# Performance work log

Measured on AMD Instinct MI355X. Metric: run time of the kernel, lower is better.

Reference implementation:

```python
import jax, jax.numpy as jnp
import numpy as np
from math import sqrt

I, H, O = 1024, 1024, 1024

def setup_inputs() -> dict:
    key = jax.random.key(0)
    ks = jax.random.split(key, 11)
    sx = sqrt(2.0 / (I + H))
    sh = sqrt(1.0 / H)
    sy = sqrt(2.0 / (H + O))
    return {
        "x": jax.random.normal(ks[0], (64, 512, I), dtype=jnp.float32),
        "W_xi": jax.random.normal(ks[1], (I, H), dtype=jnp.float32) * sx,
        "W_hi": jax.random.normal(ks[2], (H, H), dtype=jnp.float32) * sh,
        "b_i": jnp.zeros((H,), jnp.float32),
        "W_xf": jax.random.normal(ks[3], (I, H), dtype=jnp.float32) * sx,
        "W_hf": jax.random.normal(ks[4], (H, H), dtype=jnp.float32) * sh,
        "b_f": jnp.zeros((H,), jnp.float32),
        "W_xo": jax.random.normal(ks[5], (I, H), dtype=jnp.float32) * sx,
        "W_ho": jax.random.normal(ks[6], (H, H), dtype=jnp.float32) * sh,
        "b_o": jnp.zeros((H,), jnp.float32),
        "W_xc": jax.random.normal(ks[7], (I, H), dtype=jnp.float32) * sx,
        "W_hc": jax.random.normal(ks[8], (H, H), dtype=jnp.float32) * sh,
        "b_c": jnp.zeros((H,), jnp.float32),
        "W_hy": jax.random.normal(ks[9], (H, O), dtype=jnp.float32) * sy,
        "b_y": jnp.zeros((O,), jnp.float32),
    }

def reference(x, W_xi, W_hi, b_i, W_xf, W_hf, b_f, W_xo, W_ho, b_o,
              W_xc, W_hc, b_c, W_hy, b_y):
    B, T, _ = x.shape
    Hs = W_hi.shape[0]
    # Precompute all input-to-gate projections in one batched GEMM per gate.
    # Shapes: [B, T, H]
    xi = jnp.einsum('bti,ih->bth', x, W_xi) + b_i
    xf = jnp.einsum('bti,ih->bth', x, W_xf) + b_f
    xo = jnp.einsum('bti,ih->bth', x, W_xo) + b_o
    xc = jnp.einsum('bti,ih->bth', x, W_xc) + b_c

    def step(carry, inp):
        h, c = carry
        xi_t, xf_t, xo_t, xc_t = inp
        f = jax.nn.sigmoid(xf_t + h @ W_hf)
        i = jax.nn.sigmoid(xi_t + h @ W_hi)
        c_hat = jnp.tanh(xc_t + h @ W_hc)
        c_new = f * c + i * c_hat
        o = jax.nn.sigmoid(xo_t + h @ W_ho)
        h_new = o * jnp.tanh(c_new)
        return (h_new, c_new), h_new

    h0 = jnp.zeros((B, Hs), x.dtype)
    c0 = jnp.zeros((B, Hs), x.dtype)
    # scan over time: inputs stacked as [T, B, H]
    xs = (jnp.swapaxes(xi, 0, 1), jnp.swapaxes(xf, 0, 1),
          jnp.swapaxes(xo, 0, 1), jnp.swapaxes(xc, 0, 1))
    _, hs = jax.lax.scan(step, (h0, c0), xs)  # hs: [T, B, H]
    hs = jnp.swapaxes(hs, 0, 1)  # [B, T, H]
    return jnp.einsum('bth,ho->bto', hs, W_hy) + b_y
```

## Files before the change

kernel.cpp:

```cpp
#include <hip/hip_runtime.h>
#include <hip/hip_bf16.h>

typedef __attribute__((ext_vector_type(8))) short s8;
typedef __attribute__((ext_vector_type(4))) float f4;
typedef __attribute__((ext_vector_type(4))) unsigned int u4;

#define DEVI static __device__ __forceinline__

DEVI float bf2f(short u) {
  union { float f; unsigned int i; } v;
  v.i = ((unsigned int)(unsigned short)u) << 16;
  return v.f;
}
DEVI short f2bf(float f) {
  union { float f; unsigned int i; } v; v.f = f;
  unsigned int r = v.i + 0x7fffu + ((v.i >> 16) & 1u);
  return (short)(r >> 16);
}
DEVI void gload_lds16(const void* g, void* l) {
  __builtin_amdgcn_global_load_lds(
      (const __attribute__((address_space(1))) unsigned int*)g,
      (__attribute__((address_space(3))) unsigned int*)l, 16, 0, 0);
}
DEVI float sigm(float x) { return 1.f / (1.f + __expf(-x)); }

DEVI u4 load4_sc0(const void* p) {
  u4 v;
  asm volatile("global_load_dwordx4 %0, %1, off sc0" : "=v"(v) : "v"(p) : "memory");
  return v;
}
DEVI u4 load4_sc01(const void* p) {
  u4 v;
  asm volatile("global_load_dwordx4 %0, %1, off sc0 sc1" : "=v"(v) : "v"(p) : "memory");
  return v;
}
DEVI unsigned int loadw_sc0(const unsigned int* p) {
  unsigned int v;
  asm volatile("global_load_dword %0, %1, off sc0" : "=v"(v) : "v"(p) : "memory");
  asm volatile("s_waitcnt vmcnt(0)" ::: "memory");
  return v;
}
DEVI unsigned int loadw_sc01(const unsigned int* p) {
  unsigned int v;
  asm volatile("global_load_dword %0, %1, off sc0 sc1" : "=v"(v) : "v"(p) : "memory");
  asm volatile("s_waitcnt vmcnt(0)" ::: "memory");
  return v;
}
DEVI void vm0_fence() {
  asm volatile("s_waitcnt vmcnt(0)" ::: "memory");
  __builtin_amdgcn_sched_barrier(0);
}

__global__ void k_x_relayout(const float* __restrict__ in, short* __restrict__ out) {
  long idx8 = (long)blockIdx.x * blockDim.x + threadIdx.x;
  long E = idx8 * 8;
  long row = E >> 10;
  long col = E & 1023;
  long t = row >> 6, b = row & 63;
  const float* src = in + ((b << 9) + t) * 1024 + col;
  float4 a = *(const float4*)(src);
  float4 c = *(const float4*)(src + 4);
  s8 o;
  o[0] = f2bf(a.x); o[1] = f2bf(a.y); o[2] = f2bf(a.z); o[3] = f2bf(a.w);
  o[4] = f2bf(c.x); o[5] = f2bf(c.y); o[6] = f2bf(c.z); o[7] = f2bf(c.w);
  *(s8*)(out + E) = o;
}

__global__ void k_transpose_c(const float* __restrict__ src, short* __restrict__ dst) {
  __shared__ float tile[32][33];
  int n0 = blockIdx.x * 32, k0 = blockIdx.y * 32;
  int lx = threadIdx.x & 31, ly = threadIdx.x >> 5;
#pragma unroll
  for (int r = 0; r < 32; r += 8)
    tile[ly + r][lx] = src[(long)(k0 + ly + r) * 1024 + n0 + lx];
  __syncthreads();
#pragma unroll
  for (int r = 0; r < 32; r += 8)
    dst[(long)(n0 + ly + r) * 1024 + k0 + lx] = f2bf(tile[lx][ly + r]);
}

__global__ void k_bcat(const float* __restrict__ b0, const float* __restrict__ b1,
                       const float* __restrict__ b2, const float* __restrict__ b3,
                       float* __restrict__ o) {
  int i = blockIdx.x * 256 + threadIdx.x;
  int j = i & 1023;
  float v;
  switch (i >> 10) { case 0: v = b0[j]; break; case 1: v = b1[j]; break;
                     case 2: v = b2[j]; break; default: v = b3[j]; }
  o[i] = v;
}

template <typename OutT, int REMAP>
__global__ __launch_bounds__(256) void k_gemm_bt(
    const short* __restrict__ A, const short* __restrict__ Bt,
    const float* __restrict__ bias, OutT* __restrict__ C,
    int M, int N, int K) {
  __shared__ __align__(16) char As[8192];
  __shared__ __align__(16) char Bs[8192];
  const int tid = threadIdx.x;
  const int wid = tid >> 6, lane = tid & 63;
  const int lr = lane & 15, lk = lane >> 4;
  const int wy = wid >> 1, wx = wid & 1;
  const long bm = (long)blockIdx.y * 128, bn = (long)blockIdx.x * 128;
  const char* Ab = (const char*)A;
  const char* Bb = (const char*)Bt;
  f4 acc[4][4];
#pragma unroll
  for (int i = 0; i < 4; ++i)
#pragma unroll
    for (int j = 0; j < 4; ++j) acc[i][j] = f4{0.f, 0.f, 0.f, 0.f};

  for (int k0 = 0; k0 < K; k0 += 32) {
#pragma unroll
    for (int p = 0; p < 2; ++p) {
      int off = p * 4096 + tid * 16;
      int r = off >> 6, cb = off & 63;
      int sw = cb ^ ((r & 3) << 4);
      gload_lds16(Ab + ((bm + r) * K + k0) * 2 + sw, As + p * 4096 + wid * 1024);
      gload_lds16(Bb + ((bn + r) * K + k0) * 2 + sw, Bs + p * 4096 + wid * 1024);
    }
    __syncthreads();
    s8 af[4], bfr[4];
#pragma unroll
    for (int mi = 0; mi < 4; ++mi) {
      int r = wy * 64 + mi * 16 + lr;
      int x = r * 64 + lk * 16;
      af[mi] = *(const s8*)(As + (x ^ ((r & 3) << 4)));
    }
#pragma unroll
    for (int ni = 0; ni < 4; ++ni) {
      int r = wx * 64 + ni * 16 + lr;
      int x = r * 64 + lk * 16;
      bfr[ni] = *(const s8*)(Bs + (x ^ ((r & 3) << 4)));
    }
#pragma unroll
    for (int mi = 0; mi < 4; ++mi)
#pragma unroll
      for (int ni = 0; ni < 4; ++ni)
        acc[mi][ni] = __builtin_amdgcn_mfma_f32_16x16x32_bf16(af[mi], bfr[ni], acc[mi][ni], 0, 0, 0);
    __syncthreads();
  }
#pragma unroll
  for (int mi = 0; mi < 4; ++mi)
#pragma unroll
    for (int ni = 0; ni < 4; ++ni)
#pragma unroll
      for (int j = 0; j < 4; ++j) {
        long row = bm + wy * 64 + mi * 16 + lk * 4 + j;
        long col = bn + wx * 64 + ni * 16 + lr;
        float v = acc[mi][ni][j] + bias[col];
        long off;
        if constexpr (REMAP == 1) {
          off = ((row & 63) * 512 + (row >> 6)) * (long)N + col;
        } else if constexpr (REMAP == 2) {
          long tt = row >> 6, b = row & 63;
          long gg = col >> 10, u = col & 1023;
          off = (((((tt << 3) + (b >> 3)) << 5) + (u >> 5)) * 4 + gg) * 256 +
                ((b & 7) << 5) + (u & 31);
        } else {
          off = row * (long)N + col;
        }
        if constexpr (sizeof(OutT) == 2) C[off] = f2bf(v);
        else                              C[off] = v;
      }
}

__global__ __launch_bounds__(512, 2) void k_lstm_p(
    const short* __restrict__ XG,
    const short* __restrict__ Wht,
    short* __restrict__ hbuf,
    unsigned int* __restrict__ flags,
    short* __restrict__ HS) {
  __shared__ __align__(16) char hA[32768];
  __shared__ float pre[2][4][8][33];
  __shared__ int eflag;

  const int tid = threadIdx.x;
  const int wg = blockIdx.x;
  const int wid = tid >> 6, lane = tid & 63;
  const int lr = lane & 15, lk = lane >> 4;
  const int g = wid & 3, kh = wid >> 2;
  const int rb = wg & 7, ug = wg >> 3;

  if (tid == 0) eflag = 0;

  s8 wf[32];
  {
    const short* wbase = Wht + (long)(g * 1024 + ug * 32 + lr) * 1024 + kh * 512 + lk * 8;
#pragma unroll
    for (int nt = 0; nt < 2; ++nt)
#pragma unroll
      for (int kc = 0; kc < 16; ++kc)
        wf[nt * 16 + kc] = *(const s8*)(wbase + nt * 16384 + kc * 32);
  }
#pragma unroll
  for (int i = 0; i < 32; ++i) asm volatile("" : "+v"(wf[i]));

  const int srow = tid >> 6;
  {
    int zr = 8 + srow;
    int kc = lane >> 1;
    int base = kc * 1024 + zr * 64 + (lane & 1) * 32;
    int sw = ((zr + kc) & 3) << 4;
    *(u4*)(hA + (base ^ sw)) = u4{0, 0, 0, 0};
    *(u4*)(hA + ((base + 16) ^ sw)) = u4{0, 0, 0, 0};
  }

  const int erow = tid >> 5, eu = tid & 31;
  const int grow = rb * 8 + (erow & 7);
  const int gu = ug * 32 + eu;
  float c = 0.f;

  if (tid < 256) {
    short* p = &hbuf[(long)grow * 1024 + gu];
    *(volatile short*)p = 0;
    __hip_atomic_store(p, (short)0, __ATOMIC_RELAXED, __HIP_MEMORY_SCOPE_AGENT);
  }
  vm0_fence();
  __syncthreads();
  if (tid == 0) {
    unsigned int* f = &flags[(unsigned)((rb << 5) + ug) << 4];
    *(volatile unsigned int*)f = 1u;
    __hip_atomic_store(f, 1u, __ATOMIC_RELAXED, __HIP_MEMORY_SCOPE_AGENT);
  }

  short xA0 = 0, xA1 = 0, xA2 = 0, xA3 = 0, xB0, xB1, xB2, xB3;
  if (tid < 256) {
    const short* ep = XG + (long)((0 * 8 + rb) * 32 + ug) * 1024 + erow * 32 + eu;
    xA0 = ep[0]; xA1 = ep[256]; xA2 = ep[512]; xA3 = ep[768];
  }

  for (int t = 0; t < 512; ++t) {
    if (wid == 0 && lane < 32) {
      const unsigned int* f = &flags[(unsigned)((rb << 5) + lane) << 4];
      const unsigned int target = (unsigned int)(t + 1);
      int esc = eflag;
      int tries = 0;
      while (true) {
        unsigned int v = esc ? loadw_sc01(f) : loadw_sc0(f);
        if (v >= target) break;
        ++tries;
        if (tries == 8 && !esc) { esc = 1; eflag = 1; }
        if (tries > 64) __builtin_amdgcn_s_sleep(2);
        if (tries > (1 << 20)) break;
      }
    }
    __syncthreads();
    const int esc = eflag;

    {
      const char* rowp = (const char*)(hbuf + (t & 1) * 65536 +
                                       (long)(rb * 8 + srow) * 1024) + lane * 32;
      u4 v0, v1;
      if (esc) { v0 = load4_sc01(rowp); v1 = load4_sc01(rowp + 16); }
      else     { v0 = load4_sc0(rowp);  v1 = load4_sc0(rowp + 16); }
      if (tid < 256) {
        const short* ep = XG + (long)((((t + 1) & 511) * 8 + rb) * 32 + ug) * 1024 + erow * 32 + eu;
        xB0 = ep[0]; xB1 = ep[256]; xB2 = ep[512]; xB3 = ep[768];
      }
      vm0_fence();
      int kc = lane >> 1;
      int wb = kc * 1024 + srow * 64 + (lane & 1) * 32;
      int sw = ((srow + kc) & 3) << 4;
      *(u4*)(hA + (wb ^ sw)) = v0;
      *(u4*)(hA + ((wb + 16) ^ sw)) = v1;
    }
    __syncthreads();

    f4 a0{0.f, 0.f, 0.f, 0.f}, a1{0.f, 0.f, 0.f, 0.f};
#pragma unroll
    for (int kc2 = 0; kc2 < 16; ++kc2) {
      int kci = kh * 16 + kc2;
      int ad = (kci * 1024 + lr * 64 + lk * 16) ^ (((lr + kci) & 3) << 4);
      s8 ah = *(const s8*)(hA + ad);
      a0 = __builtin_amdgcn_mfma_f32_16x16x32_bf16(ah, wf[kc2], a0, 0, 0, 0);
      a1 = __builtin_amdgcn_mfma_f32_16x16x32_bf16(ah, wf[16 + kc2], a1, 0, 0, 0);
    }

    if (lk < 2) {
#pragma unroll
      for (int j = 0; j < 4; ++j) {
        pre[kh][g][lk * 4 + j][lr] = a0[j];
        pre[kh][g][lk * 4 + j][16 + lr] = a1[j];
      }
    }
    __syncthreads();

    if (tid < 256) {
      float pi = pre[0][0][erow][eu] + pre[1][0][erow][eu] + bf2f(xA0);
      float pf = pre[0][1][erow][eu] + pre[1][1][erow][eu] + bf2f(xA1);
      float po = pre[0][2][erow][eu] + pre[1][2][erow][eu] + bf2f(xA2);
      float pc = pre[0][3][erow][eu] + pre[1][3][erow][eu] + bf2f(xA3);
      float fi = sigm(pi), ff = sigm(pf), fo = sigm(po);
      float ch = tanhf(pc);
      c = ff * c + fi * ch;
      float h = fo * tanhf(c);
      short hh = f2bf(h);
      short* p = &hbuf[((t + 1) & 1) * 65536 + (long)grow * 1024 + gu];
      *(volatile short*)p = hh;
      __hip_atomic_store(p, hh, __ATOMIC_RELAXED, __HIP_MEMORY_SCOPE_AGENT);
      HS[(long)t * 65536 + (long)grow * 1024 + gu] = hh;
      xA0 = xB0; xA1 = xB1; xA2 = xB2; xA3 = xB3;
    }
    vm0_fence();
    __syncthreads();
    if (tid == 0) {
      unsigned int* f = &flags[(unsigned)((rb << 5) + ug) << 4];
      unsigned int fv = (unsigned int)(t + 2);
      *(volatile unsigned int*)f = fv;
      __hip_atomic_store(f, fv, __ATOMIC_RELAXED, __HIP_MEMORY_SCOPE_AGENT);
    }
  }
}

extern "C" void kernel_launch(void* const* d_in, const int* in_sizes, int n_in,
                              void* d_out, int out_size, void* d_ws, size_t ws_size,
                              hipStream_t stream) {
  const float* x = (const float*)d_in[0];
  const float* Wx[4] = {(const float*)d_in[1], (const float*)d_in[4], (const float*)d_in[7], (const float*)d_in[10]};
  const float* Wh[4] = {(const float*)d_in[2], (const float*)d_in[5], (const float*)d_in[8], (const float*)d_in[11]};
  const float* bg[4] = {(const float*)d_in[3], (const float*)d_in[6], (const float*)d_in[9], (const float*)d_in[12]};
  const float* Why = (const float*)d_in[13];
  const float* by  = (const float*)d_in[14];

  char* ws = (char*)d_ws;
  short* xbf  = (short*)(ws);
  short* HS   = (short*)(ws);
  short* Wxt  = (short*)(ws + 67108864);
  short* Wht  = (short*)(ws + 75497472);
  short* Whyt = (short*)(ws + 83886080);
  float* bcat = (float*)(ws + 85983232);
  short* XG   = (short*)(ws + 85999616);
  short* hbuf = (short*)(ws + 354435072);
  unsigned int* flags = (unsigned int*)(ws + 354697216);

  hipLaunchKernelGGL(k_x_relayout, dim3(16384), dim3(256), 0, stream, x, xbf);
  for (int gi = 0; gi < 4; ++gi) {
    hipLaunchKernelGGL(k_transpose_c, dim3(32, 32), dim3(256), 0, stream, Wx[gi], Wxt + (long)gi * 1048576);
    hipLaunchKernelGGL(k_transpose_c, dim3(32, 32), dim3(256), 0, stream, Wh[gi], Wht + (long)gi * 1048576);
  }
  hipLaunchKernelGGL(k_transpose_c, dim3(32, 32), dim3(256), 0, stream, Why, Whyt);
  hipLaunchKernelGGL(k_bcat, dim3(16), dim3(256), 0, stream, bg[0], bg[1], bg[2], bg[3], bcat);

  hipLaunchKernelGGL((k_gemm_bt<short, 2>), dim3(32, 256), dim3(256), 0, stream,
                     xbf, Wxt, bcat, XG, 32768, 4096, 1024);

  hipMemsetAsync(flags, 0, 16384, stream);

  {
    void* args[] = { (void*)&XG, (void*)&Wht, (void*)&hbuf, (void*)&flags, (void*)&HS };
    hipLaunchCooperativeKernel((void*)k_lstm_p, dim3(256), dim3(512), args, 0, stream);
  }

  hipLaunchKernelGGL((k_gemm_bt<float, 1>), dim3(8, 256), dim3(256), 0, stream,
                     HS, Whyt, by, (float*)d_out, 32768, 1024, 1024);
}
```

Baseline: 2.352 ms.

## Make agent-scope publishes lazy and re-publish on poll timeout; change LDS swizzle

The per-step barrier now skips the extra agent-scope atomic store of h and the flag unless an escalation flag has been set. A wave-level ballot loop polls the flags, and if polling times out it re-publishes the saved h values and flag with agent-scope atomics before retrying. The LDS swizzle for the h tile is also changed to use row>>1, which alters the bank-conflict pattern. The aim is to cut the cost of duplicate global stores on the critical recurrent path. In exchange the synchronisation protocol is more complex and relies on stores eventually becoming visible.

```diff
diff --git a/kernel.cpp b/kernel.cpp
--- a/kernel.cpp
+++ b/kernel.cpp
@@ -50,6 +50,8 @@
   asm volatile("s_waitcnt vmcnt(0)" ::: "memory");
   __builtin_amdgcn_sched_barrier(0);
 }
+
+DEVI int hswz(int row, int kc) { return (((row >> 1) + kc) & 3) << 4; }
 
 __global__ void k_x_relayout(const float* __restrict__ in, short* __restrict__ out) {
   long idx8 = (long)blockIdx.x * blockDim.x + threadIdx.x;
@@ -174,6 +176,7 @@
   __shared__ __align__(16) char hA[32768];
   __shared__ float pre[2][4][8][33];
   __shared__ int eflag;
+  __shared__ int pollok;
 
   const int tid = threadIdx.x;
   const int wg = blockIdx.x;
@@ -182,7 +185,7 @@
   const int g = wid & 3, kh = wid >> 2;
   const int rb = wg & 7, ug = wg >> 3;
 
-  if (tid == 0) eflag = 0;
+  if (tid == 0) { eflag = 0; pollok = 0; }
 
   s8 wf[32];
   {
@@ -201,7 +204,7 @@
     int zr = 8 + srow;
     int kc = lane >> 1;
     int base = kc * 1024 + zr * 64 + (lane & 1) * 32;
-    int sw = ((zr + kc) & 3) << 4;
+    int sw = hswz(zr, kc);
     *(u4*)(hA + (base ^ sw)) = u4{0, 0, 0, 0};
     *(u4*)(hA + ((base + 16) ^ sw)) = u4{0, 0, 0, 0};
   }
@@ -210,11 +213,11 @@
   const int grow = rb * 8 + (erow & 7);
   const int gu = ug * 32 + eu;
   float c = 0.f;
+  short hP0 = 0, hP1 = 0;
 
   if (tid < 256) {
     short* p = &hbuf[(long)grow * 1024 + gu];
     *(volatile short*)p = 0;
-    __hip_atomic_store(p, (short)0, __ATOMIC_RELAXED, __HIP_MEMORY_SCOPE_AGENT);
   }
   vm0_fence();
   __syncthreads();
@@ -231,21 +234,43 @@
   }
 
   for (int t = 0; t < 512; ++t) {
-    if (wid == 0 && lane < 32) {
-      const unsigned int* f = &flags[(unsigned)((rb << 5) + lane) << 4];
-      const unsigned int target = (unsigned int)(t + 1);
-      int esc = eflag;
-      int tries = 0;
-      while (true) {
-        unsigned int v = esc ? loadw_sc01(f) : loadw_sc0(f);
-        if (v >= target) break;
-        ++tries;
-        if (tries == 8 && !esc) { esc = 1; eflag = 1; }
-        if (tries > 64) __builtin_amdgcn_s_sleep(2);
-        if (tries > (1 << 20)) break;
-      }
-    }
-    __syncthreads();
+    const int target = t + 1;
+
+    int safety = 0;
+    while (true) {
+      if (wid == 0) {
+        int ok = 1;
+        if (lane < 32) {
+          const unsigned int* f = &flags[(unsigned)((rb << 5) + lane) << 4];
+          int esc = eflag;
+          ok = 0;
+          for (int r = 0; r < 256; ++r) {
+            unsigned int v = esc ? loadw_sc01(f) : loadw_sc0(f);
+            if (v >= (unsigned int)target) { ok = 1; break; }
+          }
+        }
+        unsigned long long m = __ballot(ok);
+        if (lane == 0 && m == ~0ull) pollok = target;
+      }
+      __syncthreads();
+      if (pollok >= target) break;
+      if (++safety > 4096) break;
+      if (tid == 0) eflag = 1;
+      if (tid < 256) {
+        __hip_atomic_store(&hbuf[(long)grow * 1024 + gu], hP0,
+                           __ATOMIC_RELAXED, __HIP_MEMORY_SCOPE_AGENT);
+        __hip_atomic_store(&hbuf[65536 + (long)grow * 1024 + gu], hP1,
+                           __ATOMIC_RELAXED, __HIP_MEMORY_SCOPE_AGENT);
+      }
+      vm0_fence();
+      __syncthreads();
+      if (tid == 0) {
+        unsigned int* f = &flags[(unsigned)((rb << 5) + ug) << 4];
+        *(volatile unsigned int*)f = (unsigned int)target;
+        __hip_atomic_store(f, (unsigned int)target,
+                           __ATOMIC_RELAXED, __HIP_MEMORY_SCOPE_AGENT);
+      }
+    }
     const int esc = eflag;
 
     {
@@ -261,7 +286,7 @@
       vm0_fence();
       int kc = lane >> 1;
       int wb = kc * 1024 + srow * 64 + (lane & 1) * 32;
-      int sw = ((srow + kc) & 3) << 4;
+      int sw = hswz(srow, kc);
       *(u4*)(hA + (wb ^ sw)) = v0;
       *(u4*)(hA + ((wb + 16) ^ sw)) = v1;
     }
@@ -271,7 +296,7 @@
 #pragma unroll
     for (int kc2 = 0; kc2 < 16; ++kc2) {
       int kci = kh * 16 + kc2;
-      int ad = (kci * 1024 + lr * 64 + lk * 16) ^ (((lr + kci) & 3) << 4);
+      int ad = (kci * 1024 + lr * 64 + lk * 16) ^ hswz(lr, kci);
       s8 ah = *(const s8*)(hA + ad);
       a0 = __builtin_amdgcn_mfma_f32_16x16x32_bf16(ah, wf[kc2], a0, 0, 0, 0);
       a1 = __builtin_amdgcn_mfma_f32_16x16x32_bf16(ah, wf[16 + kc2], a1, 0, 0, 0);
@@ -298,7 +323,9 @@
       short hh = f2bf(h);
       short* p = &hbuf[((t + 1) & 1) * 65536 + (long)grow * 1024 + gu];
       *(volatile short*)p = hh;
-      __hip_atomic_store(p, hh, __ATOMIC_RELAXED, __HIP_MEMORY_SCOPE_AGENT);
+      if (esc)
+        __hip_atomic_store(p, hh, __ATOMIC_RELAXED, __HIP_MEMORY_SCOPE_AGENT);
+      if ((t + 1) & 1) hP1 = hh; else hP0 = hh;
       HS[(long)t * 65536 + (long)grow * 1024 + gu] = hh;
       xA0 = xB0; xA1 = xB1; xA2 = xB2; xA3 = xB3;
     }
@@ -308,7 +335,8 @@
       unsigned int* f = &flags[(unsigned)((rb << 5) + ug) << 4];
       unsigned int fv = (unsigned int)(t + 2);
       *(volatile unsigned int*)f = fv;
-      __hip_atomic_store(f, fv, __ATOMIC_RELAXED, __HIP_MEMORY_SCOPE_AGENT);
+      if (esc)
+        __hip_atomic_store(f, fv, __ATOMIC_RELAXED, __HIP_MEMORY_SCOPE_AGENT);
     }
   }
 }
```

New measurement: 2.482 ms. 1.06x slower.

## Use per-wave flags and all-wave polling to cut block barriers in LSTM recurrence

Applied to the files above, without the earlier changes.

Replaces the single per-workgroup completion flag with four per-wave flags, so each epilogue wave publishes its own h rows right after computing them, without a block-wide barrier and a tid==0 store. Every wave now polls the flags for the row pair it needs with a wave-wide __all check, which removes the separate wave-0 spin followed by __syncthreads. The fallback to the agent-scope atomic path only triggers after many polling rounds, and in that case the previous h values are re-published. The loop is also unrolled by two to alternate the prefetched x buffers, and the LDS swizzle is changed to key on row pairs. The cost is more polling traffic, since all waves poll, plus a more fragile memory-ordering scheme that relies on plain volatile stores in the common path.

```diff
diff --git a/kernel.cpp b/kernel.cpp
--- a/kernel.cpp
+++ b/kernel.cpp
@@ -50,6 +50,8 @@
   asm volatile("s_waitcnt vmcnt(0)" ::: "memory");
   __builtin_amdgcn_sched_barrier(0);
 }
+
+DEVI int hswz(int row, int kc) { return (((row >> 1) + kc) & 3) << 4; }
 
 __global__ void k_x_relayout(const float* __restrict__ in, short* __restrict__ out) {
   long idx8 = (long)blockIdx.x * blockDim.x + threadIdx.x;
@@ -196,121 +198,147 @@
 #pragma unroll
   for (int i = 0; i < 32; ++i) asm volatile("" : "+v"(wf[i]));
 
-  const int srow = tid >> 6;
+  const int srow = wid;
+  const int ew = srow >> 1;
   {
     int zr = 8 + srow;
     int kc = lane >> 1;
     int base = kc * 1024 + zr * 64 + (lane & 1) * 32;
-    int sw = ((zr + kc) & 3) << 4;
+    int sw = hswz(zr, kc);
     *(u4*)(hA + (base ^ sw)) = u4{0, 0, 0, 0};
     *(u4*)(hA + ((base + 16) ^ sw)) = u4{0, 0, 0, 0};
   }
 
-  const int erow = tid >> 5, eu = tid & 31;
-  const int grow = rb * 8 + (erow & 7);
+  const int erow = (tid >> 5) & 7, eu = tid & 31;
+  const int grow = rb * 8 + erow;
   const int gu = ug * 32 + eu;
   float c = 0.f;
-
-  if (tid < 256) {
+  short hP0 = 0, hP1 = 0;
+
+  if (wid < 4) {
     short* p = &hbuf[(long)grow * 1024 + gu];
     *(volatile short*)p = 0;
-    __hip_atomic_store(p, (short)0, __ATOMIC_RELAXED, __HIP_MEMORY_SCOPE_AGENT);
-  }
-  vm0_fence();
+    vm0_fence();
+    if (lane == 0) {
+      unsigned int* mf = &flags[(unsigned)(((rb << 5) + ug) * 4 + wid) << 4];
+      *(volatile unsigned int*)mf = 1u;
+      __hip_atomic_store(mf, 1u, __ATOMIC_RELAXED, __HIP_MEMORY_SCOPE_AGENT);
+    }
+  }
   __syncthreads();
-  if (tid == 0) {
-    unsigned int* f = &flags[(unsigned)((rb << 5) + ug) << 4];
-    *(volatile unsigned int*)f = 1u;
-    __hip_atomic_store(f, 1u, __ATOMIC_RELAXED, __HIP_MEMORY_SCOPE_AGENT);
-  }
-
-  short xA0 = 0, xA1 = 0, xA2 = 0, xA3 = 0, xB0, xB1, xB2, xB3;
-  if (tid < 256) {
+
+  short xE[4], xO[4];
+  if (wid < 4) {
     const short* ep = XG + (long)((0 * 8 + rb) * 32 + ug) * 1024 + erow * 32 + eu;
-    xA0 = ep[0]; xA1 = ep[256]; xA2 = ep[512]; xA3 = ep[768];
-  }
-
-  for (int t = 0; t < 512; ++t) {
-    if (wid == 0 && lane < 32) {
-      const unsigned int* f = &flags[(unsigned)((rb << 5) + lane) << 4];
-      const unsigned int target = (unsigned int)(t + 1);
-      int esc = eflag;
-      int tries = 0;
-      while (true) {
-        unsigned int v = esc ? loadw_sc01(f) : loadw_sc0(f);
-        if (v >= target) break;
-        ++tries;
-        if (tries == 8 && !esc) { esc = 1; eflag = 1; }
-        if (tries > 64) __builtin_amdgcn_s_sleep(2);
-        if (tries > (1 << 20)) break;
-      }
-    }
-    __syncthreads();
-    const int esc = eflag;
-
-    {
-      const char* rowp = (const char*)(hbuf + (t & 1) * 65536 +
-                                       (long)(rb * 8 + srow) * 1024) + lane * 32;
-      u4 v0, v1;
-      if (esc) { v0 = load4_sc01(rowp); v1 = load4_sc01(rowp + 16); }
-      else     { v0 = load4_sc0(rowp);  v1 = load4_sc0(rowp + 16); }
-      if (tid < 256) {
-        const short* ep = XG + (long)((((t + 1) & 511) * 8 + rb) * 32 + ug) * 1024 + erow * 32 + eu;
-        xB0 = ep[0]; xB1 = ep[256]; xB2 = ep[512]; xB3 = ep[768];
-      }
-      vm0_fence();
-      int kc = lane >> 1;
-      int wb = kc * 1024 + srow * 64 + (lane & 1) * 32;
-      int sw = ((srow + kc) & 3) << 4;
-      *(u4*)(hA + (wb ^ sw)) = v0;
-      *(u4*)(hA + ((wb + 16) ^ sw)) = v1;
-    }
-    __syncthreads();
-
-    f4 a0{0.f, 0.f, 0.f, 0.f}, a1{0.f, 0.f, 0.f, 0.f};
-#pragma unroll
-    for (int kc2 = 0; kc2 < 16; ++kc2) {
-      int kci = kh * 16 + kc2;
-      int ad = (kci * 1024 + lr * 64 + lk * 16) ^ (((lr + kci) & 3) << 4);
-      s8 ah = *(const s8*)(hA + ad);
-      a0 = __builtin_amdgcn_mfma_f32_16x16x32_bf16(ah, wf[kc2], a0, 0, 0, 0);
-      a1 = __builtin_amdgcn_mfma_f32_16x16x32_bf16(ah, wf[16 + kc2], a1, 0, 0, 0);
-    }
-
-    if (lk < 2) {
-#pragma unroll
-      for (int j = 0; j < 4; ++j) {
-        pre[kh][g][lk * 4 + j][lr] = a0[j];
-        pre[kh][g][lk * 4 + j][16 + lr] = a1[j];
-      }
-    }
-    __syncthreads();
-
-    if (tid < 256) {
-      float pi = pre[0][0][erow][eu] + pre[1][0][erow][eu] + bf2f(xA0);
-      float pf = pre[0][1][erow][eu] + pre[1][1][erow][eu] + bf2f(xA1);
-      float po = pre[0][2][erow][eu] + pre[1][2][erow][eu] + bf2f(xA2);
-      float pc = pre[0][3][erow][eu] + pre[1][3][erow][eu] + bf2f(xA3);
-      float fi = sigm(pi), ff = sigm(pf), fo = sigm(po);
-      float ch = tanhf(pc);
-      c = ff * c + fi * ch;
-      float h = fo * tanhf(c);
-      short hh = f2bf(h);
-      short* p = &hbuf[((t + 1) & 1) * 65536 + (long)grow * 1024 + gu];
-      *(volatile short*)p = hh;
-      __hip_atomic_store(p, hh, __ATOMIC_RELAXED, __HIP_MEMORY_SCOPE_AGENT);
-      HS[(long)t * 65536 + (long)grow * 1024 + gu] = hh;
-      xA0 = xB0; xA1 = xB1; xA2 = xB2; xA3 = xB3;
-    }
-    vm0_fence();
-    __syncthreads();
-    if (tid == 0) {
-      unsigned int* f = &flags[(unsigned)((rb << 5) + ug) << 4];
-      unsigned int fv = (unsigned int)(t + 2);
-      *(volatile unsigned int*)f = fv;
-      __hip_atomic_store(f, fv, __ATOMIC_RELAXED, __HIP_MEMORY_SCOPE_AGENT);
-    }
-  }
+    xE[0] = ep[0]; xE[1] = ep[256]; xE[2] = ep[512]; xE[3] = ep[768];
+  }
+
+#define LSTM_STEP(T, XA, XB)                                                    \
+  {                                                                             \
+    const int t_ = (T);                                                         \
+    const unsigned int target = (unsigned int)(t_ + 1);                         \
+    {                        \
+      const unsigned int* fp =                                                  \
+          &flags[(unsigned)(((rb << 5) + (lane & 31)) * 4 + ew) << 4];          \
+      int esc = *(volatile int*)&eflag;                                         \
+      int rounds = 0;                                                           \
+      while (true) {                                                            \
+        unsigned int v = esc ? loadw_sc01(fp) : loadw_sc0(fp);                  \
+        if (__all((int)(v >= target))) break;                                   \
+        ++rounds;                                                               \
+        if (rounds >= 4096 && (rounds & 4095) == 0) {                           \
+          if (lane == 0) eflag = 1;                                             \
+          esc = 1;                                                              \
+          if (wid < 4) {                  \
+            __hip_atomic_store(&hbuf[(long)grow * 1024 + gu], hP0,              \
+                               __ATOMIC_RELAXED, __HIP_MEMORY_SCOPE_AGENT);     \
+            __hip_atomic_store(&hbuf[65536 + (long)grow * 1024 + gu], hP1,      \
+                               __ATOMIC_RELAXED, __HIP_MEMORY_SCOPE_AGENT);     \
+            vm0_fence();                                                        \
+            if (lane == 0) {                                                    \
+              unsigned int* mf =                                                \
+                  &flags[(unsigned)(((rb << 5) + ug) * 4 + wid) << 4];          \
+              __hip_atomic_store(mf, target, __ATOMIC_RELAXED,                  \
+                                 __HIP_MEMORY_SCOPE_AGENT);                     \
+            }                                                                   \
+          }                                                                     \
+        } else {                                                                \
+          esc = *(volatile int*)&eflag;                                         \
+        }                                                                       \
+        if (rounds > (1 << 20)) break;                                          \
+      }                                                                         \
+    }                                                                           \
+    const int esc_ = *(volatile int*)&eflag;                                    \
+    {                    \
+      const char* rowp = (const char*)(hbuf + (t_ & 1) * 65536 +                \
+                                       (long)(rb * 8 + srow) * 1024) +          \
+                         lane * 32;                                             \
+      u4 v0, v1;                                                                \
+      if (esc_) { v0 = load4_sc01(rowp); v1 = load4_sc01(rowp + 16); }          \
+      else      { v0 = load4_sc0(rowp);  v1 = load4_sc0(rowp + 16); }           \
+      vm0_fence();                                                              \
+      int kc_ = lane >> 1;                                                      \
+      int wb = kc_ * 1024 + srow * 64 + (lane & 1) * 32;                        \
+      int sw = hswz(srow, kc_);                                                 \
+      *(u4*)(hA + (wb ^ sw)) = v0;                                              \
+      *(u4*)(hA + ((wb + 16) ^ sw)) = v1;                                       \
+    }                                                                           \
+    __syncthreads();                                          \
+    f4 a0{0.f, 0.f, 0.f, 0.f}, a1{0.f, 0.f, 0.f, 0.f};                          \
+    _Pragma("unroll")                                                           \
+    for (int kc2 = 0; kc2 < 16; ++kc2) {                                        \
+      int kci = kh * 16 + kc2;                                                  \
+      int ad = (kci * 1024 + lr * 64 + lk * 16) ^ hswz(lr, kci);                \
+      s8 ah = *(const s8*)(hA + ad);                                            \
+      a0 = __builtin_amdgcn_mfma_f32_16x16x32_bf16(ah, wf[kc2], a0, 0, 0, 0);   \
+      a1 = __builtin_amdgcn_mfma_f32_16x16x32_bf16(ah, wf[16 + kc2], a1, 0, 0, 0); \
+    }                                                                           \
+    if (lk < 2) {                                                               \
+      _Pragma("unroll")                                                         \
+      for (int j = 0; j < 4; ++j) {                                             \
+        pre[kh][g][lk * 4 + j][lr] = a0[j];                                     \
+        pre[kh][g][lk * 4 + j][16 + lr] = a1[j];                                \
+      }                                                                         \
+    }                                                                           \
+    __syncthreads();                                         \
+    if (wid < 4) {                                                              \
+      float pi = pre[0][0][erow][eu] + pre[1][0][erow][eu] + bf2f(XA[0]);       \
+      float pf = pre[0][1][erow][eu] + pre[1][1][erow][eu] + bf2f(XA[1]);       \
+      float po = pre[0][2][erow][eu] + pre[1][2][erow][eu] + bf2f(XA[2]);       \
+      float pc = pre[0][3][erow][eu] + pre[1][3][erow][eu] + bf2f(XA[3]);       \
+      float fi = sigm(pi), ff = sigm(pf), fo = sigm(po);                        \
+      float ch = tanhf(pc);                                                     \
+      c = ff * c + fi * ch;                                                     \
+      float h = fo * tanhf(c);                                                  \
+      short hh = f2bf(h);                                                       \
+      short* p = &hbuf[((t_ + 1) & 1) * 65536 + (long)grow * 1024 + gu];        \
+      *(volatile short*)p = hh;                                                 \
+      if (esc_)                                                                 \
+        __hip_atomic_store(p, hh, __ATOMIC_RELAXED, __HIP_MEMORY_SCOPE_AGENT);  \
+      if ((t_ + 1) & 1) hP1 = hh; else hP0 = hh;                                \
+      vm0_fence();                      \
+      if (lane == 0) {                                                          \
+        unsigned int* mf = &flags[(unsigned)(((rb << 5) + ug) * 4 + wid) << 4]; \
+        *(volatile unsigned int*)mf = (unsigned int)(t_ + 2);                   \
+        if (esc_)                                                               \
+          __hip_atomic_store(mf, (unsigned int)(t_ + 2), __ATOMIC_RELAXED,      \
+                             __HIP_MEMORY_SCOPE_AGENT);                         \
+      }                                                                         \
+      HS[(long)t_ * 65536 + (long)grow * 1024 + gu] = hh;                       \
+      {     \
+        int tn = (t_ + 1) & 511;                                                \
+        const short* ep = XG + (long)((tn * 8 + rb) * 32 + ug) * 1024 +         \
+                          erow * 32 + eu;                                       \
+        XB[0] = ep[0]; XB[1] = ep[256]; XB[2] = ep[512]; XB[3] = ep[768];       \
+      }                                                                         \
+    }                                                                           \
+  }
+
+  for (int t2 = 0; t2 < 512; t2 += 2) {
+    LSTM_STEP(t2, xE, xO);
+    LSTM_STEP(t2 + 1, xO, xE);
+  }
+#undef LSTM_STEP
 }
 
 extern "C" void kernel_launch(void* const* d_in, const int* in_sizes, int n_in,
@@ -345,7 +373,7 @@
   hipLaunchKernelGGL((k_gemm_bt<short, 2>), dim3(32, 256), dim3(256), 0, stream,
                      xbf, Wxt, bcat, XG, 32768, 4096, 1024);
 
-  hipMemsetAsync(flags, 0, 16384, stream);
+  hipMemsetAsync(flags, 0, 65536, stream);
 
   {
     void* args[] = { (void*)&XG, (void*)&Wht, (void*)&hbuf, (void*)&flags, (void*)&HS };
```

Result: slower. 4.494 ms (+91.0%).
